# Performance work log

Hardware: AMD Instinct MI355X
Metric: run time of the kernel (lower is better)

## Reference

```python
import jax, jax.numpy as jnp
import numpy as np
from jax.scipy.special import logsumexp

B, L, M, D = 8192, 1024, 128, 2  # batch, hilbert.size, bond dim, local_size
MACHINE_POW = 2


def setup_inputs() -> dict:
    key = jax.random.key(0)
    k1, k2 = jax.random.split(key)
    # configurations in the zero-magnetization sector: each row is a permutation
    # of L//2 zeros and L//2 ones (constrained HomogeneousHilbert)
    base = jnp.tile(jnp.arange(D, dtype=jnp.int32), L // D)  # (L,)
    inputs = jax.vmap(lambda k: jax.random.permutation(k, base))(jax.random.split(k1, B))
    # variational parameters epsilon: (local_size, M, size); centered at 1 so the
    # length-L multiplicative cache chain stays in fp32 range
    epsilon = 1.0 + 0.02 * jax.random.normal(k2, (D, M, L), dtype=jnp.float32)
    return {"inputs": inputs, "epsilon": epsilon}


def _conditionals(inputs, epsilon):
    # inputs: (B, L) int in [0, D); epsilon: (D, M, L)
    Bn, Ln = inputs.shape
    Dn, Mn, _ = epsilon.shape
    half = Ln // 2

    def scan_fun(carry, index):
        cache, n_spins = carry                       # (B, D, M), (B, D)
        prev = inputs[:, (index - 1) % Ln]           # (B,) previous-site state
        params_i = epsilon[:, :, index]              # (D, M)
        # irregular gather: cache[b, prev[b], :]
        gathered = jnp.take_along_axis(cache, prev[:, None, None], axis=1)[:, 0, :]  # (B, M)
        prods = params_i[None, :, :] * gathered[:, None, :]  # (B, D, M)
        log_psi = jnp.sum(prods, axis=-1)            # (B, D) sum over bond dim
        n_spins = jnp.where(index > 0,
                            n_spins + jax.nn.one_hot(prev, Dn, dtype=jnp.int32),
                            n_spins)
        # zero-magnetization renormalization: -inf once a local state is exhausted
        renorm = jnp.log(jnp.heaviside((half - n_spins).astype(log_psi.dtype), 0.0))
        return (prods, n_spins), log_psi + renorm

    cache0 = jnp.ones((Bn, Dn, Mn), epsilon.dtype)
    n0 = jnp.zeros((Bn, Dn), jnp.int32)
    _, log_psi = jax.lax.scan(scan_fun, (cache0, n0), jnp.arange(Ln))
    return jnp.transpose(log_psi, (1, 0, 2))  # (B, L, D)


def reference(inputs, epsilon):
    lp = _conditionals(inputs, epsilon)  # (B, L, D)
    # normalize conditionals over local states (machine_pow = 2)
    lp = lp - (1.0 / MACHINE_POW) * logsumexp(MACHINE_POW * lp, axis=-1, keepdims=True)
    # pick the log-conditional of the actual configuration at each site
    sel = jnp.take_along_axis(lp, inputs[:, :, None], axis=2)[:, :, 0]  # (B, L)
    # n_symm = 1 (default apply_symmetries): symmetrized logsumexp is identity
    return jnp.sum(sel, axis=1)  # (B,) log_psi
```

## Files before the change

kernel.cpp:

```cpp
#include <hip/hip_runtime.h>
#include <hip/hip_fp16.h>

typedef unsigned long long u64;
typedef unsigned int uint32;
typedef short short8 __attribute__((ext_vector_type(8)));
typedef float f32x4 __attribute__((ext_vector_type(4)));
typedef _Float16 h2 __attribute__((ext_vector_type(2)));

#define B_N 8192
#define L_N 1024
#define M_N 128
#define C_N 16
#define CH_N 64
#define HALF_N 512

#define OFF_W16  0
#define OFF_R16  0x40000
#define OFF_BITS 0x80000
#define OFF_LR   0x180000
#define OFF_RQ   0x1C0000
#define OFF_T    0x21C0000

#define PACK_BLK 2048
#define PACK_IT  16
#define EPS_BLK  32
#define ZERO_BLK 32

__device__ __forceinline__ unsigned short f32_bf16(float f) {
    union { float f; unsigned u; } x; x.f = f;
    unsigned u = x.u + 0x7FFFu + ((x.u >> 16) & 1u);
    return (unsigned short)(u >> 16);
}

__device__ __forceinline__ float fdot2(h2 a, h2 b, float c) {
#if __has_builtin(__builtin_amdgcn_fdot2)
    return __builtin_amdgcn_fdot2(a, b, c, false);
#else
    return (float)a[0] * (float)b[0] + (float)a[1] * (float)b[1] + c;
#endif
}

__device__ __forceinline__ uint32 fas_u(float f) { union { float f; uint32 u; } x; x.f = f; return x.u; }
__device__ __forceinline__ float uas_f(uint32 u) { union { uint32 u; float f; } x; x.u = u; return x.f; }

__device__ __forceinline__ float exp2_n(float x) {
#if __has_builtin(__builtin_amdgcn_exp2f)
    return __builtin_amdgcn_exp2f(x);
#else
    return exp2f(x);
#endif
}
__device__ __forceinline__ float log2_n(float x) {
#if __has_builtin(__builtin_amdgcn_logf)
    return __builtin_amdgcn_logf(x);
#else
    return __log2f(x);
#endif
}
__device__ __forceinline__ uint32 bfe1(uint32 v, int off) {
#if __has_builtin(__builtin_amdgcn_sbfe)
    return (uint32)__builtin_amdgcn_sbfe((int)v, off, 1);
#else
    return (uint32)((int)(v << (31 - off)) >> 31);
#endif
}

template<int CTRL>
__device__ __forceinline__ float dpp_add(float x, float y) {
    union { float f; int i; } a, r;
    a.f = y;
    r.i = __builtin_amdgcn_update_dpp(0, a.i, CTRL, 0xF, 0xF, true);
    return x + r.f;
}

union HU { uint32 u; __half2 hh; h2 v2; };

__global__ __launch_bounds__(256) void k_prep(const int* __restrict__ inp,
        const float* __restrict__ eps, u64* __restrict__ bits,
        _Float16* __restrict__ w16, _Float16* __restrict__ r16,
        unsigned short* __restrict__ lrT, float* __restrict__ out) {
    int bid = blockIdx.x;
    if (bid < PACK_BLK) {
        int g = bid * 256 + threadIdx.x;
        const int stride = PACK_BLK * 256;
        #pragma unroll 4
        for (int it = 0; it < PACK_IT; ++it) {
            int v = inp[g];
            u64 m = __ballot(v != 0);
            if ((threadIdx.x & 63) == 0) bits[g >> 6] = m;
            g += stride;
        }
        return;
    }
    bid -= PACK_BLK;
    if (bid < EPS_BLK) {
        int wid = threadIdx.x >> 6, lane = threadIdx.x & 63;
        int m = bid * 4 + wid;
        const float* e0 = eps + (size_t)m * L_N + lane * 16;
        const float* e1 = eps + (size_t)(M_N + m) * L_N + lane * 16;
        float a[16], b[16];
        #pragma unroll
        for (int j = 0; j < 16; j += 4) {
            *(float4*)&a[j] = *(const float4*)&e0[j];
            *(float4*)&b[j] = *(const float4*)&e1[j];
        }
        float local = 1.f;
        #pragma unroll
        for (int j = 0; j < 16; ++j) local *= a[j];
        float sc = local;
        #pragma unroll
        for (int d = 1; d < 64; d <<= 1) {
            float up = __shfl_up(sc, d);
            if (lane >= d) sc *= up;
        }
        float prev = __shfl_up(sc, 1);
        float E = (lane == 0) ? 1.f : prev;
        int i0 = lane * 16;
        #pragma unroll
        for (int j = 0; j < 16; ++j) {
            float rat = b[j] / a[j];
            w16[(size_t)(i0 + j) * M_N + m] = (_Float16)(E * (a[j] - b[j]));
            r16[(size_t)(i0 + j) * M_N + m] = (_Float16)(rat - 1.f);
            lrT[(size_t)m * L_N + i0 + j] = f32_bf16(__log2f(rat));
            E *= a[j];
        }
        return;
    }
    bid -= EPS_BLK;
    if (bid < ZERO_BLK) {
        out[bid * 256 + threadIdx.x] = 0.f;
    }
}

__global__ __launch_bounds__(256) void k_slog2(const u64* __restrict__ bits,
        const unsigned short* __restrict__ lrT, _Float16* __restrict__ Rq,
        int* __restrict__ T) {
    if (blockIdx.x >= 1024) {
        int b = (blockIdx.x - 1024) * 256 + threadIdx.x;
        const u64* brow = bits + (size_t)b * 16;
        int n1 = 0, n0 = 0, Tv = 1024;
        for (int wd = 0; wd < 16; ++wd) {
            u64 x = brow[wd];
            int pc = __popcll(x);
            if (n1 + pc < HALF_N && n0 + (64 - pc) < HALF_N) {
                n1 += pc; n0 += 64 - pc;
                continue;
            }
            int found = 0;
            for (int k = 0; k < 64; ++k) {
                if (n1 >= HALF_N || n0 >= HALF_N) { Tv = wd * 64 + k; found = 1; break; }
                int sb = (int)((x >> k) & 1);
                n1 += sb; n0 += 1 - sb;
            }
            if (!found) Tv = (wd + 1) * 64;
            break;
        }
        T[b] = Tv;
        return;
    }
    int btile = blockIdx.x >> 1;
    int half = blockIdx.x & 1;
    int wid = threadIdx.x >> 6, lane = threadIdx.x & 63;
    int col = lane & 15, quad = lane >> 4;
    int m = (half * 4 + wid) * 16 + col;
    int b_row = btile * 16 + col;
    const u64* brow = bits + (size_t)b_row * 16;
    const unsigned short* lrow = lrT + (size_t)m * L_N;

    f32x4 cum = (f32x4){0.f, 0.f, 0.f, 0.f};

    for (int c = 0; c < C_N; ++c) {
        #pragma unroll
        for (int reg = 0; reg < 4; ++reg) {
            int b = btile * 16 + quad * 4 + reg;
            Rq[((size_t)c * B_N + b) * M_N + m] = (_Float16)exp2_n(cum[reg]);
        }
        u64 wv = brow[c];
        short8 a0, a1;
        #pragma unroll
        for (int j = 0; j < 8; ++j) {
            a0[j] = (short)((((wv >> (quad * 8 + j)) & 1) != 0) ? 0x3F80 : 0);
            a1[j] = (short)((((wv >> (32 + quad * 8 + j)) & 1) != 0) ? 0x3F80 : 0);
        }
        const unsigned short* bp = lrow + c * 64 + quad * 8;
        union { uint4 u; short8 s; } bf0, bf1;
        bf0.u = *(const uint4*)bp;
        bf1.u = *(const uint4*)(bp + 32);
        cum = __builtin_amdgcn_mfma_f32_16x16x32_bf16(a0, bf0.s, cum, 0, 0, 0);
        cum = __builtin_amdgcn_mfma_f32_16x16x32_bf16(a1, bf1.s, cum, 0, 0, 0);
    }
}

__global__ __launch_bounds__(256, 2) void k_main(const u64* __restrict__ bits,
        const _Float16* __restrict__ w16, const _Float16* __restrict__ r16,
        const _Float16* __restrict__ Rq, const int* __restrict__ T,
        float* __restrict__ out) {
    __shared__ _Float16 wbuf[CH_N * M_N];
    __shared__ _Float16 rbuf[CH_N * M_N];
    int c = blockIdx.x & (C_N - 1);
    int bblk = blockIdx.x >> 4;
    int lane = threadIdx.x & 63, wid = threadIdx.x >> 6;
    int s = lane & 7, grp = lane >> 3;
    int q = s & 3;
    int b0 = bblk * 128 + wid * 32 + grp * 4;

    {
        const uint4* sw = (const uint4*)(w16 + (size_t)c * CH_N * M_N);
        const uint4* sr = (const uint4*)(r16 + (size_t)c * CH_N * M_N);
        uint4* dw = (uint4*)wbuf; uint4* dr = (uint4*)rbuf;
        #pragma unroll
        for (int t = 0; t < 4; ++t) {
            dw[threadIdx.x + t * 256] = sw[threadIdx.x + t * 256];
            dr[threadIdx.x + t * 256] = sr[threadIdx.x + t * 256];
        }
    }

    HU R2[4][8];
    u64 wb[4];
    #pragma unroll
    for (int k = 0; k < 4; ++k) {
        int b = b0 + (q ^ k);
        union { uint4 v[2]; uint32 w[8]; } P;
        const uint4* src = (const uint4*)(Rq + ((size_t)c * B_N + b) * M_N + s * 16);
        P.v[0] = src[0]; P.v[1] = src[1];
        #pragma unroll
        for (int j = 0; j < 8; ++j) R2[k][j].u = P.w[j];
        wb[k] = bits[(size_t)b * 16 + c];
    }
    int Tb = T[b0 + q];

    __syncthreads();

    const float LOG2E2 = 2.885390082f;
    const float NHL2 = -0.3465735903f;
    float sum = 0.f;
    #pragma unroll
    for (int h = 0; h < 2; ++h) {
        uint32 wh[4];
        #pragma unroll
        for (int k = 0; k < 4; ++k) wh[k] = (uint32)(wb[k] >> (h * 32));
        uint32 ows = ~wh[0];
        int rel = Tb - (c * CH_N + h * 32);
        uint32 vmask = (rel <= 0) ? 0u : ((rel >= 32) ? 0xFFFFFFFFu : ((1u << rel) - 1u));

        for (int tt = 0; tt < 32; ++tt) {
            int base = (h * 32 + tt) * M_N + s * 16;
            union { uint4 q4[2]; uint32 w[8]; h2 v2[8]; } W, Rm;
            W.q4[0] = *(const uint4*)&wbuf[base];
            W.q4[1] = *((const uint4*)&wbuf[base] + 1);
            Rm.q4[0] = *(const uint4*)&rbuf[base];
            Rm.q4[1] = *((const uint4*)&rbuf[base] + 1);

            float d[4];
            #pragma unroll
            for (int k = 0; k < 4; ++k) {
                float acc = 0.f;
                #pragma unroll
                for (int j = 0; j < 8; ++j) acc = fdot2(R2[k][j].v2, W.v2[j], acc);
                d[k] = acc;
            }
            float xa = dpp_add<0xB1>(d[0], d[1]);
            float xb = dpp_add<0xB1>(d[2], d[3]);
            float uD = dpp_add<0x4E>(xa, xb);
            uD = dpp_add<0x104>(uD, uD);

            uint32 sgn = bfe1(ows, tt) & 0x80000000u;
            float y = uas_f(fas_u(uD) ^ sgn);
            float contr = NHL2 * log2_n(1.f + exp2_n(LOG2E2 * y));
            sum += uas_f(fas_u(contr) & bfe1(vmask, tt));

            #pragma unroll
            for (int k = 0; k < 4; ++k) {
                uint32 msk = bfe1(wh[k], tt);
                #pragma unroll
                for (int j = 0; j < 8; ++j) {
                    HU sel; sel.u = Rm.w[j] & msk;
                    R2[k][j].v2 += sel.v2 * R2[k][j].v2;
                }
            }
        }
    }
    if (s < 4) atomicAdd(&out[b0 + s], sum);
}

extern "C" void kernel_launch(void* const* d_in, const int* in_sizes, int n_in,
                              void* d_out, int out_size, void* d_ws, size_t ws_size,
                              hipStream_t stream) {
    const int*   inputs  = (const int*)d_in[0];
    const float* epsilon = (const float*)d_in[1];
    float* out = (float*)d_out;

    char* ws = (char*)d_ws;
    _Float16* w16 = (_Float16*)(ws + OFF_W16);
    _Float16* r16 = (_Float16*)(ws + OFF_R16);
    u64*   bits   = (u64*)  (ws + OFF_BITS);
    unsigned short* lrT = (unsigned short*)(ws + OFF_LR);
    _Float16* Rq  = (_Float16*)(ws + OFF_RQ);
    int*   T      = (int*)  (ws + OFF_T);

    k_prep<<<PACK_BLK + EPS_BLK + ZERO_BLK, 256, 0, stream>>>(
        inputs, epsilon, bits, w16, r16, lrT, out);
    k_slog2<<<1024 + 32, 256, 0, stream>>>(bits, lrT, Rq, T);
    k_main<<<(B_N / 128) * C_N, 256, 0, stream>>>(bits, w16, r16, Rq, T, out);
}
```

Measured before the change: 171.3 us.

## Process eight batch rows per lane group in k_main with 128-thread blocks

Each 8-lane group of k_main now handles 8 batch rows instead of 4, and blocks shrink from 256 to 128 threads. Each LDS load of the weight and R rows is therefore reused across twice as many rows, and the DPP reduction yields two outputs per step. The cache update also switches to an explicit __hfma2, and the inner loop is unrolled by 2. In exchange, register use roughly doubles (64 packed R values per lane), which lowers occupancy and may spill. Each block now needs twice as many LDS fill iterations per thread.

Result: slower. 178.8 us (+4.4%).

```diff
diff --git a/kernel.cpp b/kernel.cpp
--- a/kernel.cpp
+++ b/kernel.cpp
@@ -191,7 +191,7 @@
     }
 }
 
-__global__ __launch_bounds__(256, 2) void k_main(const u64* __restrict__ bits,
+__global__ __launch_bounds__(128) void k_main(const u64* __restrict__ bits,
         const _Float16* __restrict__ w16, const _Float16* __restrict__ r16,
         const _Float16* __restrict__ Rq, const int* __restrict__ T,
         float* __restrict__ out) {
@@ -201,25 +201,24 @@
     int bblk = blockIdx.x >> 4;
     int lane = threadIdx.x & 63, wid = threadIdx.x >> 6;
     int s = lane & 7, grp = lane >> 3;
-    int q = s & 3;
-    int b0 = bblk * 128 + wid * 32 + grp * 4;
+    int b0 = bblk * 128 + wid * 64 + grp * 8;
 
     {
         const uint4* sw = (const uint4*)(w16 + (size_t)c * CH_N * M_N);
         const uint4* sr = (const uint4*)(r16 + (size_t)c * CH_N * M_N);
         uint4* dw = (uint4*)wbuf; uint4* dr = (uint4*)rbuf;
         #pragma unroll
-        for (int t = 0; t < 4; ++t) {
-            dw[threadIdx.x + t * 256] = sw[threadIdx.x + t * 256];
-            dr[threadIdx.x + t * 256] = sr[threadIdx.x + t * 256];
-        }
-    }
-
-    HU R2[4][8];
-    u64 wb[4];
+        for (int t = 0; t < 8; ++t) {
+            dw[threadIdx.x + t * 128] = sw[threadIdx.x + t * 128];
+            dr[threadIdx.x + t * 128] = sr[threadIdx.x + t * 128];
+        }
+    }
+
+    HU R2[8][8];
+    u64 wb[8];
     #pragma unroll
-    for (int k = 0; k < 4; ++k) {
-        int b = b0 + (q ^ k);
+    for (int k = 0; k < 8; ++k) {
+        int b = b0 + (s ^ k);
         union { uint4 v[2]; uint32 w[8]; } P;
         const uint4* src = (const uint4*)(Rq + ((size_t)c * B_N + b) * M_N + s * 16);
         P.v[0] = src[0]; P.v[1] = src[1];
@@ -227,22 +226,27 @@
         for (int j = 0; j < 8; ++j) R2[k][j].u = P.w[j];
         wb[k] = bits[(size_t)b * 16 + c];
     }
-    int Tb = T[b0 + q];
+    int Tb_lo = T[b0 + (s & 3)];
+    int Tb_hi = T[b0 + 4 + (s & 3)];
 
     __syncthreads();
 
     const float LOG2E2 = 2.885390082f;
     const float NHL2 = -0.3465735903f;
-    float sum = 0.f;
+    float sum_lo = 0.f, sum_hi = 0.f;
     #pragma unroll
     for (int h = 0; h < 2; ++h) {
-        uint32 wh[4];
-        #pragma unroll
-        for (int k = 0; k < 4; ++k) wh[k] = (uint32)(wb[k] >> (h * 32));
-        uint32 ows = ~wh[0];
-        int rel = Tb - (c * CH_N + h * 32);
-        uint32 vmask = (rel <= 0) ? 0u : ((rel >= 32) ? 0xFFFFFFFFu : ((1u << rel) - 1u));
-
+        uint32 wh[8];
+        #pragma unroll
+        for (int k = 0; k < 8; ++k) wh[k] = (uint32)(wb[k] >> (h * 32));
+        uint32 ows_lo = ~wh[0];
+        uint32 ows_hi = ~wh[4];
+        int rel_lo = Tb_lo - (c * CH_N + h * 32);
+        int rel_hi = Tb_hi - (c * CH_N + h * 32);
+        uint32 vm_lo = (rel_lo <= 0) ? 0u : ((rel_lo >= 32) ? 0xFFFFFFFFu : ((1u << rel_lo) - 1u));
+        uint32 vm_hi = (rel_hi <= 0) ? 0u : ((rel_hi >= 32) ? 0xFFFFFFFFu : ((1u << rel_hi) - 1u));
+
+        #pragma unroll 2
         for (int tt = 0; tt < 32; ++tt) {
             int base = (h * 32 + tt) * M_N + s * 16;
             union { uint4 q4[2]; uint32 w[8]; h2 v2[8]; } W, Rm;
@@ -251,36 +255,47 @@
             Rm.q4[0] = *(const uint4*)&rbuf[base];
             Rm.q4[1] = *((const uint4*)&rbuf[base] + 1);
 
-            float d[4];
+            float d[8];
             #pragma unroll
-            for (int k = 0; k < 4; ++k) {
+            for (int k = 0; k < 8; ++k) {
                 float acc = 0.f;
                 #pragma unroll
                 for (int j = 0; j < 8; ++j) acc = fdot2(R2[k][j].v2, W.v2[j], acc);
                 d[k] = acc;
             }
-            float xa = dpp_add<0xB1>(d[0], d[1]);
-            float xb = dpp_add<0xB1>(d[2], d[3]);
-            float uD = dpp_add<0x4E>(xa, xb);
-            uD = dpp_add<0x104>(uD, uD);
-
-            uint32 sgn = bfe1(ows, tt) & 0x80000000u;
-            float y = uas_f(fas_u(uD) ^ sgn);
-            float contr = NHL2 * log2_n(1.f + exp2_n(LOG2E2 * y));
-            sum += uas_f(fas_u(contr) & bfe1(vmask, tt));
+            float a0 = dpp_add<0xB1>(d[0], d[1]);
+            float a2 = dpp_add<0xB1>(d[2], d[3]);
+            float a4 = dpp_add<0xB1>(d[4], d[5]);
+            float a6 = dpp_add<0xB1>(d[6], d[7]);
+            float u0 = dpp_add<0x4E>(a0, a2);
+            float u4 = dpp_add<0x4E>(a4, a6);
+            float D_lo = dpp_add<0x104>(u0, u4);
+            float D_hi = dpp_add<0x104>(u4, u0);
+
+            uint32 sg_lo = bfe1(ows_lo, tt) & 0x80000000u;
+            float y_lo = uas_f(fas_u(D_lo) ^ sg_lo);
+            float ct_lo = NHL2 * log2_n(1.f + exp2_n(LOG2E2 * y_lo));
+            sum_lo += uas_f(fas_u(ct_lo) & bfe1(vm_lo, tt));
+            uint32 sg_hi = bfe1(ows_hi, tt) & 0x80000000u;
+            float y_hi = uas_f(fas_u(D_hi) ^ sg_hi);
+            float ct_hi = NHL2 * log2_n(1.f + exp2_n(LOG2E2 * y_hi));
+            sum_hi += uas_f(fas_u(ct_hi) & bfe1(vm_hi, tt));
 
             #pragma unroll
-            for (int k = 0; k < 4; ++k) {
+            for (int k = 0; k < 8; ++k) {
                 uint32 msk = bfe1(wh[k], tt);
                 #pragma unroll
                 for (int j = 0; j < 8; ++j) {
                     HU sel; sel.u = Rm.w[j] & msk;
-                    R2[k][j].v2 += sel.v2 * R2[k][j].v2;
+                    R2[k][j].hh = __hfma2(sel.hh, R2[k][j].hh, R2[k][j].hh);
                 }
             }
         }
     }
-    if (s < 4) atomicAdd(&out[b0 + s], sum);
+    if (s < 4) {
+        atomicAdd(&out[b0 + s], sum_lo);
+        atomicAdd(&out[b0 + 4 + s], sum_hi);
+    }
 }
 
 extern "C" void kernel_launch(void* const* d_in, const int* in_sizes, int n_in,
@@ -301,5 +316,5 @@
     k_prep<<<PACK_BLK + EPS_BLK + ZERO_BLK, 256, 0, stream>>>(
         inputs, epsilon, bits, w16, r16, lrT, out);
     k_slog2<<<1024 + 32, 256, 0, stream>>>(bits, lrT, Rq, T);
-    k_main<<<(B_N / 128) * C_N, 256, 0, stream>>>(bits, w16, r16, Rq, T, out);
-}
+    k_main<<<(B_N / 128) * C_N, 128, 0, stream>>>(bits, w16, r16, Rq, T, out);
+}
```
